# Optimization experiments

Measured on AMD Instinct MI355X. Metric: run time of the kernel, lower is better.

## Reference

```python
import jax, jax.numpy as jnp
import numpy as np

EPS = 1e-5
NUM_HEADS = 8


def _conv(x, w, pad, dil=1, groups=1, b=None):
    y = jax.lax.conv_general_dilated(
        x, w, (1, 1), pad, rhs_dilation=(dil, dil),
        dimension_numbers=('NCHW', 'OIHW', 'NCHW'), feature_group_count=groups)
    if b is not None:
        y = y + b[None, :, None, None]
    return y


def _bn_relu(x, gamma, beta):
    # BatchNorm2d in training mode: batch statistics over (N,H,W) per channel
    mu = x.mean(axis=(0, 2, 3), keepdims=True)
    var = x.var(axis=(0, 2, 3), keepdims=True)
    y = (x - mu) / jnp.sqrt(var + EPS) * gamma[None, :, None, None] + beta[None, :, None, None]
    return jax.nn.relu(y)


def _ln(x, w, b):
    # WithBias LayerNorm over channel dim (to_3d makes C the last axis)
    mu = x.mean(axis=1, keepdims=True)
    var = x.var(axis=1, keepdims=True)
    return (x - mu) / jnp.sqrt(var + EPS) * w[None, :, None, None] + b[None, :, None, None]


def _l2n(t):
    # torch F.normalize: x / max(||x||_2, 1e-12)
    return t / jnp.maximum(jnp.linalg.norm(t, axis=-1, keepdims=True), 1e-12)


def _forward(x, ln_w, ln_b, wd1, gd1, bd1, wd2, gd2, bd2, wd3, gd3, bd3,
             w_out1, w1, b1, w2, b2, w3, b3, w4, b4, w5, b5, w6, b6, w_out2):
    B, C, H, W = x.shape
    head, ch = NUM_HEADS, C // NUM_HEADS
    x1 = _ln(x, ln_w, ln_b)
    # dilated dense-conv branch (DConv2d = conv -> BN -> ReLU), dilations [1,6,12]
    x11 = _bn_relu(_conv(x, wd1, ((0, 0), (0, 0))), gd1, bd1)
    x12 = _bn_relu(_conv(x, wd2, ((6, 6), (6, 6)), dil=6), gd2, bd2)
    x13 = _bn_relu(_conv(x, wd3, ((12, 12), (12, 12)), dil=12), gd3, bd3)
    out2 = _conv(x11 + x12 + x13, w_out1, ((0, 0), (0, 0))) + x
    # six depthwise conv branches, summed
    att = (_conv(x1, w1, ((0, 0), (2, 2)), groups=C, b=b1)
           + _conv(x1, w2, ((2, 2), (0, 0)), groups=C, b=b2)
           + _conv(x1, w3, ((0, 0), (0, 0)), groups=C, b=b3)
           + _conv(x1, w4, ((1, 1), (1, 1)), groups=C, b=b4)
           + _conv(x1, w5, ((0, 0), (3, 3)), groups=C, b=b5)
           + _conv(x1, w6, ((3, 3), (0, 0)), groups=C, b=b6))
    out1 = _conv(att, w_out2, ((0, 0), (0, 0)))

    def r_hwc(t):  # b (head c) h w -> b head h (w c)
        return t.reshape(B, head, ch, H, W).transpose(0, 1, 3, 4, 2).reshape(B, head, H, W * ch)

    def r_whc(t):  # b (head c) h w -> b head w (h c)
        return t.reshape(B, head, ch, H, W).transpose(0, 1, 4, 3, 2).reshape(B, head, W, H * ch)

    k1 = _l2n(r_hwc(out1))
    v1 = r_hwc(out1)
    k2 = _l2n(r_whc(out2))
    v2 = r_whc(out2)
    q2 = _l2n(r_whc(out1))
    q1 = _l2n(r_whc(out2))
    A1 = jax.nn.softmax(q1 @ jnp.swapaxes(k1, -2, -1), axis=-1)  # [B,head,W,H]
    out3 = A1 @ v1 + q1
    A2 = jax.nn.softmax(q2 @ jnp.swapaxes(k2, -2, -1), axis=-1)
    out4 = A2 @ v2 + q2
    # b head h (w c) -> b (head c) h w
    o3 = out3.reshape(B, head, H, W, ch).transpose(0, 1, 4, 2, 3).reshape(B, C, H, W)
    # b head w (h c) -> b (head c) h w
    o4 = out4.reshape(B, head, W, H, ch).transpose(0, 1, 4, 3, 2).reshape(B, C, H, W)
    return _conv(o3, w_out2, ((0, 0), (0, 0))) + _conv(o4, w_out2, ((0, 0), (0, 0))) + x


def setup_inputs() -> dict:
    key = jax.random.key(0)
    ks = jax.random.split(key, 16)
    B, C, H, W = 8, 128, 128, 128

    def rn(k, shape, s):
        return jax.random.normal(k, shape, jnp.float32) * s

    inp = {}
    inp['x'] = jax.random.normal(ks[0], (B, C, H, W), jnp.float32)
    inp['ln_w'] = jnp.ones((C,), jnp.float32)
    inp['ln_b'] = jnp.zeros((C,), jnp.float32)
    inp['wd1'] = rn(ks[1], (C, C, 1, 1), 0.1)
    inp['gd1'] = jnp.ones((C,), jnp.float32)
    inp['bd1'] = jnp.zeros((C,), jnp.float32)
    inp['wd2'] = rn(ks[2], (C, C, 3, 3), 0.04)
    inp['gd2'] = jnp.ones((C,), jnp.float32)
    inp['bd2'] = jnp.zeros((C,), jnp.float32)
    inp['wd3'] = rn(ks[3], (C, C, 3, 3), 0.04)
    inp['gd3'] = jnp.ones((C,), jnp.float32)
    inp['bd3'] = jnp.zeros((C,), jnp.float32)
    inp['w_out1'] = rn(ks[4], (C, C, 1, 1), 0.09)
    inp['w1'] = rn(ks[5], (C, 1, 1, 5), 0.3)
    inp['b1'] = jnp.zeros((C,), jnp.float32)
    inp['w2'] = rn(ks[6], (C, 1, 5, 1), 0.3)
    inp['b2'] = jnp.zeros((C,), jnp.float32)
    inp['w3'] = rn(ks[7], (C, 1, 1, 1), 0.5)
    inp['b3'] = jnp.zeros((C,), jnp.float32)
    inp['w4'] = rn(ks[8], (C, 1, 3, 3), 0.2)
    inp['b4'] = jnp.zeros((C,), jnp.float32)
    inp['w5'] = rn(ks[9], (C, 1, 1, 7), 0.25)
    inp['b5'] = jnp.zeros((C,), jnp.float32)
    inp['w6'] = rn(ks[10], (C, 1, 7, 1), 0.25)
    inp['b6'] = jnp.zeros((C,), jnp.float32)
    inp['w_out2'] = rn(ks[11], (C, C, 1, 1), 0.09)
    return inp


def reference(x, ln_w, ln_b, wd1, gd1, bd1, wd2, gd2, bd2, wd3, gd3, bd3,
              w_out1, w1, b1, w2, b2, w3, b3, w4, b4, w5, b5, w6, b6, w_out2):
    return _forward(x, ln_w, ln_b, wd1, gd1, bd1, wd2, gd2, bd2, wd3, gd3, bd3,
                    w_out1, w1, b1, w2, b2, w3, b3, w4, b4, w5, b5, w6, b6, w_out2)
```

## Files before the change

kernel.cpp:

```cpp
#include <hip/hip_runtime.h>

#define Bb 8
#define Cc 128
#define Hh 128
#define Ww 128
#define HW 16384
#define CHW (Cc*HW)
#define NHW (Bb*HW)
#define CH 16
#define EPS 1e-5f
#define NSLICE 16

typedef __attribute__((ext_vector_type(8))) short bf16x8;
typedef __attribute__((ext_vector_type(4))) float f32x4;

static __device__ __forceinline__ short f2b(float f) {
  unsigned u = __float_as_uint(f);
  unsigned lsb = (u >> 16) & 1;
  return (short)((u + 0x7fffu + lsb) >> 16);
}
static __device__ __forceinline__ float b2f(short s) {
  return __uint_as_float(((unsigned)(unsigned short)s) << 16);
}

static __device__ __forceinline__ void stats_epilogue(
    float* __restrict__ statp, f32x4 acc[4][4], int co0, int quad, int lm)
{
  statp += (blockIdx.x & (NSLICE-1)) * 768;
  #pragma unroll
  for (int i = 0; i < 4; ++i) {
    f32x4 s = acc[i][0] + acc[i][1] + acc[i][2] + acc[i][3];
    f32x4 q = acc[i][0]*acc[i][0] + acc[i][1]*acc[i][1]
            + acc[i][2]*acc[i][2] + acc[i][3]*acc[i][3];
    #pragma unroll
    for (int m = 1; m < 16; m <<= 1) {
      #pragma unroll
      for (int e = 0; e < 4; ++e) {
        s[e] += __shfl_xor(s[e], m);
        q[e] += __shfl_xor(q[e], m);
      }
    }
    if (lm == 0) {
      int co = co0 + i*16 + quad*4;
      #pragma unroll
      for (int e = 0; e < 4; ++e) {
        atomicAdd(&statp[co + e], s[e]);
        atomicAdd(&statp[128 + co + e], q[e]);
      }
    }
  }
}

__global__ __launch_bounds__(256) void k_ln(const float* __restrict__ x,
    const float* __restrict__ g, const float* __restrict__ be,
    float* __restrict__ y)
{
  int p = blockIdx.x*256 + threadIdx.x;
  int b = p >> 14, hw = p & 16383;
  const float* xp = x + (long)b*CHW + hw;
  float s = 0.f, q = 0.f;
  for (int c = 0; c < Cc; ++c) { float v = xp[c*HW]; s += v; q += v*v; }
  float mu = s * (1.f/Cc);
  float var = q * (1.f/Cc) - mu*mu;
  float rstd = rsqrtf(var + EPS);
  float* yp = y + (long)b*CHW + hw;
  for (int c = 0; c < Cc; ++c) {
    float v = xp[c*HW];
    yp[c*HW] = (v - mu) * rstd * g[c] + be[c];
  }
}

__global__ __launch_bounds__(256) void k_reorg3b(const float* __restrict__ Wt, short* __restrict__ out)
{
  int idx = blockIdx.x*256 + threadIdx.x;
  int tap = idx >> 14, r = idx & 16383;
  out[idx] = f2b(Wt[r*9 + tap]);
}

__global__ __launch_bounds__(256) void k_cast(const float* __restrict__ in, short* __restrict__ out)
{
  int i = blockIdx.x*256 + threadIdx.x;
  out[i] = f2b(in[i]);
}

__global__ __launch_bounds__(256) void k_zero(float* p, int n)
{
  int i = blockIdx.x*256 + threadIdx.x;
  if (i < n) p[i] = 0.f;
}

__global__ __launch_bounds__(256) void k_nhwc(const float* __restrict__ in, short* __restrict__ out)
{
  __shared__ float Ls[32][33];
  int bid = blockIdx.x;
  int hwt = bid & 511, c4 = (bid>>9)&3, b = bid>>11;
  int hw0 = hwt << 5, c0 = c4 << 5;
  int t = threadIdx.x;
  int hl = t & 31, cl = t >> 5;
  const float* p = in + (long)b*CHW + hw0;
  for (int r = cl; r < 32; r += 8)
    Ls[r][hl] = p[(long)(c0+r)*HW + hl];
  __syncthreads();
  short* q = out + ((long)b*HW + hw0)*Cc + c0;
  int ccl = t & 31, hl0 = t >> 5;
  for (int r = hl0; r < 32; r += 8)
    q[(long)r*Cc + ccl] = f2b(Ls[ccl][r]);
}

__global__ __launch_bounds__(256,2) void k_mconv(const short* __restrict__ X,
    const short* __restrict__ W, float* __restrict__ Y, int k3, int dil,
    float* __restrict__ statp)
{
  __shared__ short Ws[128*136];
  __shared__ short Xs[152*136];
  int b = blockIdx.x >> 7, h = blockIdx.x & 127;
  int t = threadIdx.x;
  int wave = t >> 6, lane = t & 63;
  int co0 = (wave >> 1) << 6, sp0 = (wave & 1) << 6;
  int lm = lane & 15, quad = lane >> 4;
  f32x4 acc[4][4];
  #pragma unroll
  for (int i = 0; i < 4; ++i)
    #pragma unroll
    for (int j = 0; j < 4; ++j) acc[i][j] = (f32x4){0.f,0.f,0.f,0.f};
  int half = k3 >> 1;

  {
    f32x4 z = {0.f,0.f,0.f,0.f};
    for (int i = t; i < 408; i += 256) {
      int r = i / 17, o = i - r*17;
      int row = r < 12 ? r : r + 128;
      *(f32x4*)(Xs + row*136 + o*8) = z;
    }
  }

  for (int kh = 0; kh < k3; ++kh) {
    int hs = h + (kh - half)*dil;
    if ((unsigned)hs >= (unsigned)Hh) continue;
    __syncthreads();
    {
      const short* xr = X + ((long)(b*Hh + hs)*Ww)*Cc;
      #pragma unroll
      for (int it = 0; it < 8; ++it) {
        int i = t + it*256;
        int row = i >> 4, off = (i & 15) << 3;
        *(f32x4*)(Xs + (12 + row)*136 + off) = *(const f32x4*)(xr + (long)row*Cc + off);
      }
    }
    for (int kw = 0; kw < k3; ++kw) {
      int dw = (kw - half)*dil;
      if (kw) __syncthreads();
      {
        const short* wt = W + (kh*k3 + kw)*16384;
        #pragma unroll
        for (int it = 0; it < 8; ++it) {
          int i = t + it*256;
          int row = i >> 4, off = (i & 15) << 3;
          *(f32x4*)(Ws + row*136 + off) = *(const f32x4*)(wt + (long)row*128 + off);
        }
      }
      __syncthreads();
      int xrow0 = 12 + dw + sp0;
      for (int kc = 0; kc < 4; ++kc) {
        int k0 = kc << 5;
        bf16x8 af[4], bfr[4];
        #pragma unroll
        for (int i = 0; i < 4; ++i)
          af[i] = *(const bf16x8*)(Ws + (co0 + i*16 + lm)*136 + k0 + quad*8);
        #pragma unroll
        for (int j = 0; j < 4; ++j)
          bfr[j] = *(const bf16x8*)(Xs + (xrow0 + j*16 + lm)*136 + k0 + quad*8);
        #pragma unroll
        for (int i = 0; i < 4; ++i)
          #pragma unroll
          for (int j = 0; j < 4; ++j)
            acc[i][j] = __builtin_amdgcn_mfma_f32_16x16x32_bf16(af[i], bfr[j], acc[i][j], 0, 0, 0);
      }
    }
  }
  float* yb = Y + ((long)(b*Hh + h)*Ww)*Cc;
  #pragma unroll
  for (int i = 0; i < 4; ++i) {
    int co = co0 + i*16 + quad*4;
    #pragma unroll
    for (int j = 0; j < 4; ++j) {
      int wc = sp0 + j*16 + lm;
      *(f32x4*)(yb + (long)wc*Cc + co) = acc[i][j];
    }
  }
  if (statp) stats_epilogue(statp, acc, co0, quad, lm);
}

__global__ __launch_bounds__(256,4) void k_mconv1(const short* __restrict__ X,
    const short* __restrict__ W, const float* __restrict__ res,
    float* __restrict__ Y, int nhwc, float* __restrict__ statp)
{
  __shared__ short Ws[128*136];
  int b = blockIdx.x >> 7, h = blockIdx.x & 127;
  int t = threadIdx.x;
  int wave = t >> 6, lane = t & 63;
  int co0 = (wave >> 1) << 6, sp0 = (wave & 1) << 6;
  int lm = lane & 15, quad = lane >> 4;
  #pragma unroll
  for (int it = 0; it < 8; ++it) {
    int i = t + it*256;
    int row = i >> 4, off = (i & 15) << 3;
    *(f32x4*)(Ws + row*136 + off) = *(const f32x4*)(W + (long)row*128 + off);
  }
  f32x4 acc[4][4];
  #pragma unroll
  for (int i = 0; i < 4; ++i)
    #pragma unroll
    for (int j = 0; j < 4; ++j) acc[i][j] = (f32x4){0.f,0.f,0.f,0.f};
  const short* xr = X + ((long)(b*Hh + h)*Ww)*Cc;
  __syncthreads();
  #pragma unroll
  for (int kc = 0; kc < 4; ++kc) {
    int k0 = kc << 5;
    bf16x8 af[4], bfr[4];
    #pragma unroll
    for (int j = 0; j < 4; ++j)
      bfr[j] = *(const bf16x8*)(xr + (long)(sp0 + j*16 + lm)*Cc + k0 + quad*8);
    #pragma unroll
    for (int i = 0; i < 4; ++i)
      af[i] = *(const bf16x8*)(Ws + (co0 + i*16 + lm)*136 + k0 + quad*8);
    #pragma unroll
    for (int i = 0; i < 4; ++i)
      #pragma unroll
      for (int j = 0; j < 4; ++j)
        acc[i][j] = __builtin_amdgcn_mfma_f32_16x16x32_bf16(af[i], bfr[j], acc[i][j], 0, 0, 0);
  }
  if (nhwc) {
    float* yb = Y + ((long)(b*Hh + h)*Ww)*Cc;
    #pragma unroll
    for (int i = 0; i < 4; ++i) {
      int co = co0 + i*16 + quad*4;
      #pragma unroll
      for (int j = 0; j < 4; ++j) {
        int wc = sp0 + j*16 + lm;
        *(f32x4*)(yb + (long)wc*Cc + co) = acc[i][j];
      }
    }
    if (statp) stats_epilogue(statp, acc, co0, quad, lm);
  } else {
    __syncthreads();
    float* scr = (float*)Ws + wave*320;
    int co_l = lane >> 2, wq = (lane & 3) << 2;
    #pragma unroll
    for (int i = 0; i < 4; ++i) {
      #pragma unroll
      for (int j = 0; j < 4; ++j) {
        #pragma unroll
        for (int r = 0; r < 4; ++r)
          scr[(quad*4 + r)*20 + lm] = acc[i][j][r];
        f32x4 vv = *(f32x4*)(scr + co_l*20 + wq);
        int co = co0 + i*16 + co_l;
        int wc = sp0 + j*16 + wq;
        long idx = ((long)(b*Cc + co)*Hh + h)*Ww + wc;
        if (res) vv += *(const f32x4*)(res + idx);
        *(f32x4*)(Y + idx) = vv;
      }
    }
  }
}

__global__ __launch_bounds__(128) void k_bnfin(const float* __restrict__ stats,
    const float* __restrict__ g1, const float* __restrict__ be1,
    const float* __restrict__ g2, const float* __restrict__ be2,
    const float* __restrict__ g3, const float* __restrict__ be3,
    float* __restrict__ so)
{
  int c = threadIdx.x;
  const float inv = 1.f/(float)NHW;
  const float* gs[3] = {g1, g2, g3};
  const float* bs[3] = {be1, be2, be3};
  #pragma unroll
  for (int tsel = 0; tsel < 3; ++tsel) {
    float su = 0.f, qu = 0.f;
    for (int sl = 0; sl < NSLICE; ++sl) {
      su += stats[sl*768 + tsel*256 + c];
      qu += stats[sl*768 + tsel*256 + 128 + c];
    }
    float mu = su*inv;
    float var = qu*inv - mu*mu;
    float s = rsqrtf(var + EPS)*gs[tsel][c];
    so[tsel*256 + c] = s;
    so[tsel*256 + 128 + c] = bs[tsel][c] - mu*s;
  }
}

__global__ __launch_bounds__(256) void k_bnapply(const float* __restrict__ y1,
    const float* __restrict__ y2, const float* __restrict__ y3,
    const float* __restrict__ so, short* __restrict__ sb)
{
  long e = ((long)blockIdx.x*256 + threadIdx.x) * 8;
  int c = (int)(e & 127);
  f32x4 s1a = *(const f32x4*)(so + c),        s1b = *(const f32x4*)(so + c + 4);
  f32x4 o1a = *(const f32x4*)(so + 128 + c),  o1b = *(const f32x4*)(so + 132 + c);
  f32x4 s2a = *(const f32x4*)(so + 256 + c),  s2b = *(const f32x4*)(so + 260 + c);
  f32x4 o2a = *(const f32x4*)(so + 384 + c),  o2b = *(const f32x4*)(so + 388 + c);
  f32x4 s3a = *(const f32x4*)(so + 512 + c),  s3b = *(const f32x4*)(so + 516 + c);
  f32x4 o3a = *(const f32x4*)(so + 640 + c),  o3b = *(const f32x4*)(so + 644 + c);
  f32x4 v1a = *(const f32x4*)(y1 + e), v1b = *(const f32x4*)(y1 + e + 4);
  f32x4 v2a = *(const f32x4*)(y2 + e), v2b = *(const f32x4*)(y2 + e + 4);
  f32x4 v3a = *(const f32x4*)(y3 + e), v3b = *(const f32x4*)(y3 + e + 4);
  float r[8];
  #pragma unroll
  for (int k = 0; k < 4; ++k) {
    r[k] = fmaxf(fmaf(v1a[k], s1a[k], o1a[k]), 0.f)
         + fmaxf(fmaf(v2a[k], s2a[k], o2a[k]), 0.f)
         + fmaxf(fmaf(v3a[k], s3a[k], o3a[k]), 0.f);
    r[4+k] = fmaxf(fmaf(v1b[k], s1b[k], o1b[k]), 0.f)
           + fmaxf(fmaf(v2b[k], s2b[k], o2b[k]), 0.f)
           + fmaxf(fmaf(v3b[k], s3b[k], o3b[k]), 0.f);
  }
  int4 o;
  o.x = ((int)(unsigned short)f2b(r[1])<<16) | (unsigned short)f2b(r[0]);
  o.y = ((int)(unsigned short)f2b(r[3])<<16) | (unsigned short)f2b(r[2]);
  o.z = ((int)(unsigned short)f2b(r[5])<<16) | (unsigned short)f2b(r[4]);
  o.w = ((int)(unsigned short)f2b(r[7])<<16) | (unsigned short)f2b(r[6]);
  *(int4*)(sb + e) = o;
}

__global__ __launch_bounds__(256) void k_dw2(const float* __restrict__ X,
    const float* __restrict__ w1, const float* __restrict__ b1,
    const float* __restrict__ w2, const float* __restrict__ b2,
    const float* __restrict__ w3, const float* __restrict__ b3,
    const float* __restrict__ w4, const float* __restrict__ b4,
    const float* __restrict__ w5, const float* __restrict__ b5,
    const float* __restrict__ w6, const float* __restrict__ b6,
    float* __restrict__ Y)
{
  __shared__ float Ls[38][136];
  int bid = blockIdx.x;
  int tile = bid & 3, plane = bid >> 2;
  int c = plane & 127;
  int h0 = tile << 5;
  int t = threadIdx.x;

  float hcoef[7], vcoef[7], k9[9];
  #pragma unroll
  for (int d = 0; d < 7; ++d) { hcoef[d] = w5[c*7+d]; vcoef[d] = w6[c*7+d]; }
  #pragma unroll
  for (int d = 1; d < 6; ++d) { hcoef[d] += w1[c*5+d-1]; vcoef[d] += w2[c*5+d-1]; }
  hcoef[3] += w3[c];
  #pragma unroll
  for (int k = 0; k < 9; ++k) k9[k] = w4[c*9+k];
  float bias = b1[c]+b2[c]+b3[c]+b4[c]+b5[c]+b6[c];

  const float* xp = X + (long)plane*HW;

  f32x4* lz = (f32x4*)&Ls[0][0];
  for (int i = t; i < 1292; i += 256) lz[i] = (f32x4){0.f,0.f,0.f,0.f};
  __syncthreads();
  for (int i = t; i < 1216; i += 256) {
    int r = i >> 5, cg = (i & 31) << 2;
    int h = h0 - 3 + r;
    if ((unsigned)h < 128u)
      *(f32x4*)&Ls[r][4 + cg] = *(const f32x4*)(xp + h*128 + cg);
  }
  __syncthreads();

  int g = t & 31, rs = t >> 5;
  int w0 = g << 2;
  float* Yp = Y + (long)plane*HW;

  for (int ro = 0; ro < 4; ++ro) {
    int lr = rs + (ro << 3);
    int R = lr + 3;
    f32x4 a0 = *(const f32x4*)&Ls[R][w0];
    f32x4 a1 = *(const f32x4*)&Ls[R][w0+4];
    f32x4 a2 = *(const f32x4*)&Ls[R][w0+8];
    f32x4 u0 = *(const f32x4*)&Ls[R-1][w0];
    f32x4 u1 = *(const f32x4*)&Ls[R-1][w0+4];
    f32x4 u2 = *(const f32x4*)&Ls[R-1][w0+8];
    f32x4 d0 = *(const f32x4*)&Ls[R+1][w0];
    f32x4 d1 = *(const f32x4*)&Ls[R+1][w0+4];
    f32x4 d2 = *(const f32x4*)&Ls[R+1][w0+8];
    f32x4 v3u = *(const f32x4*)&Ls[R-3][w0+4];
    f32x4 v2u = *(const f32x4*)&Ls[R-2][w0+4];
    f32x4 v2d = *(const f32x4*)&Ls[R+2][w0+4];
    f32x4 v3d = *(const f32x4*)&Ls[R+3][w0+4];

    float cr[12], ur[12], dr[12];
    #pragma unroll
    for (int k = 0; k < 4; ++k) {
      cr[k] = a0[k]; cr[4+k] = a1[k]; cr[8+k] = a2[k];
      ur[k] = u0[k]; ur[4+k] = u1[k]; ur[8+k] = u2[k];
      dr[k] = d0[k]; dr[4+k] = d1[k]; dr[8+k] = d2[k];
    }

    f32x4 o;
    #pragma unroll
    for (int j = 0; j < 4; ++j) {
      float acc = bias;
      #pragma unroll
      for (int d = 0; d < 7; ++d) acc = fmaf(hcoef[d], cr[j+d+1], acc);
      acc = fmaf(vcoef[0], v3u[j], acc);
      acc = fmaf(vcoef[1], v2u[j], acc);
      acc = fmaf(vcoef[2], ur[j+4], acc);
      acc = fmaf(vcoef[3], cr[j+4], acc);
      acc = fmaf(vcoef[4], dr[j+4], acc);
      acc = fmaf(vcoef[5], v2d[j], acc);
      acc = fmaf(vcoef[6], v3d[j], acc);
      #pragma unroll
      for (int kw = 0; kw < 3; ++kw) {
        acc = fmaf(k9[kw],   ur[j+3+kw], acc);
        acc = fmaf(k9[3+kw], cr[j+3+kw], acc);
        acc = fmaf(k9[6+kw], dr[j+3+kw], acc);
      }
      o[j] = acc;
    }
    *(f32x4*)(Yp + (h0 + lr)*128 + w0) = o;
  }
}

__global__ __launch_bounds__(256) void k_normh(const float* __restrict__ out1, float* __restrict__ invn)
{
  __shared__ float red[256];
  int bid = blockIdx.x;
  int h = bid & 127; int bh = bid >> 7;
  int b = bh >> 3, hd = bh & 7;
  const float* p = out1 + ((long)(b*Cc + hd*CH)*Hh + h)*Ww;
  float s = 0.f;
  for (int e = threadIdx.x; e < 2048; e += 256) {
    int c = e >> 7, w = e & 127;
    float v = p[(long)c*HW + w];
    s += v*v;
  }
  red[threadIdx.x] = s; __syncthreads();
  for (int st = 128; st > 0; st >>= 1) {
    if (threadIdx.x < st) red[threadIdx.x] += red[threadIdx.x+st];
    __syncthreads();
  }
  if (threadIdx.x == 0) invn[bid] = 1.f/fmaxf(sqrtf(red[0]), 1e-12f);
}

__global__ __launch_bounds__(256) void k_normw_part(const float* __restrict__ out1,
    const float* __restrict__ out2, float* __restrict__ acc1, float* __restrict__ acc2)
{
  __shared__ float red[4][256];
  int bid = blockIdx.x;
  int c = bid & 15, bh = (bid >> 4) & 63, tsel = bid >> 10;
  int b = bh >> 3, hd = bh & 7;
  const float* p = (tsel ? out2 : out1) + (long)(b*Cc + hd*CH + c)*HW;
  int t = threadIdx.x;
  const float4* p4 = (const float4*)p;
  float s0 = 0.f, s1 = 0.f, s2 = 0.f, s3 = 0.f;
  for (int i = t; i < 4096; i += 256) {
    float4 v = p4[i];
    s0 += v.x*v.x; s1 += v.y*v.y; s2 += v.z*v.z; s3 += v.w*v.w;
  }
  red[0][t] = s0; red[1][t] = s1; red[2][t] = s2; red[3][t] = s3;
  __syncthreads();
  if (t < 128) {
    int j = t >> 5;
    int g = t & 31;
    float tot = 0.f;
    #pragma unroll
    for (int r = 0; r < 8; ++r) tot += red[j][g + r*32];
    atomicAdd((tsel ? acc2 : acc1) + bh*128 + g*4 + j, tot);
  }
}

__global__ __launch_bounds__(256) void k_finw(float* __restrict__ p)
{
  int i = blockIdx.x*256 + threadIdx.x;
  float v = p[i];
  p[i] = 1.f/fmaxf(sqrtf(v), 1e-12f);
}

__global__ __launch_bounds__(256) void k_t12(const float* __restrict__ out1,
    const float* __restrict__ out2, short* __restrict__ out1T, short* __restrict__ out2T)
{
  __shared__ float Ls[32][33];
  int bid = blockIdx.x;
  int wt = bid&3, ht=(bid>>2)&3, c=(bid>>4)&127, b=(bid>>11)&7, src=bid>>14;
  const float* in = (src ? out2 : out1) + (long)(b*128+c)*16384;
  short* outp = (src ? out2T : out1T) + ((long)(b*8 + (c>>4))*128)*2048 + (c&15)*128;
  int h0 = ht*32, w0 = wt*32;
  int t = threadIdx.x, li = t&31, r0 = t>>5;
  for (int r = r0; r < 32; r += 8)
    Ls[r][li] = in[(h0+r)*128 + w0 + li];
  __syncthreads();
  for (int r = r0; r < 32; r += 8)
    outp[(long)(w0+r)*2048 + h0 + li] = f2b(Ls[li][r]);
}

__global__ __launch_bounds__(256) void k_h12(const float* __restrict__ out1,
    const float* __restrict__ out2, short* __restrict__ out1H, short* __restrict__ out2H)
{
  int bid = blockIdx.x;
  int src = bid >> 13;
  long e = ((long)(bid & 8191)*256 + threadIdx.x) * 8;
  const float* p;
  short* dst;
  if (src) { p = out2 + e; dst = out2H + e; }
  else {
    int c = (int)((e>>7)&15), h = (int)((e>>11)&127), hd=(int)((e>>18)&7), b=(int)(e>>21);
    int pp = (int)(e & 127);
    p = out1 + (((long)(b*128 + hd*16 + c)*128 + h)*128 + pp);
    dst = out1H + e;
  }
  int4 o;
  o.x = ((int)(unsigned short)f2b(p[1])<<16) | (unsigned short)f2b(p[0]);
  o.y = ((int)(unsigned short)f2b(p[3])<<16) | (unsigned short)f2b(p[2]);
  o.z = ((int)(unsigned short)f2b(p[5])<<16) | (unsigned short)f2b(p[4]);
  o.w = ((int)(unsigned short)f2b(p[7])<<16) | (unsigned short)f2b(p[6]);
  *(int4*)dst = o;
}

__global__ __launch_bounds__(256) void k_attnS_m(
    const short* __restrict__ out1T, const short* __restrict__ out2T,
    const short* __restrict__ out1H,
    const float* __restrict__ invn1h, const float* __restrict__ invn1w,
    const float* __restrict__ invn2w,
    short* __restrict__ A1b, short* __restrict__ A2b)
{
  __shared__ short As[128*72];
  __shared__ short Bs[128*72];
  int bid = blockIdx.x;
  int type = bid >> 6, bh = bid & 63;
  const short* Aop = (type ? out1T : out2T) + (long)bh*262144;
  const short* Bop = (type ? out2T : out1H) + (long)bh*262144;
  const float* invrow = (type ? invn1w : invn2w) + bh*128;
  const float* invcol = (type ? invn2w : invn1h) + bh*128;
  short* Aout = (type ? A2b : A1b) + (long)bh*16384;
  int t = threadIdx.x;
  int wave = t >> 6, lane = t & 63, lm = lane & 15, quad = lane >> 4;
  int m0 = wave << 5;
  f32x4 acc[2][8];
  #pragma unroll
  for (int i = 0; i < 2; ++i)
    #pragma unroll
    for (int j = 0; j < 8; ++j) acc[i][j] = (f32x4){0.f,0.f,0.f,0.f};
  for (int kc = 0; kc < 32; ++kc) {
    int k0 = kc << 6;
    __syncthreads();
    #pragma unroll
    for (int i = 0; i < 4; ++i) {
      int e = t + i*256;
      int row = e >> 3, off = (e & 7) << 3;
      *(float4*)(As + row*72 + off) = *(const float4*)(Aop + (long)row*2048 + k0 + off);
      *(float4*)(Bs + row*72 + off) = *(const float4*)(Bop + (long)row*2048 + k0 + off);
    }
    __syncthreads();
    #pragma unroll
    for (int ks = 0; ks < 64; ks += 32) {
      bf16x8 af[2], bfj[8];
      #pragma unroll
      for (int i = 0; i < 2; ++i)
        af[i] = *(const bf16x8*)(As + (m0 + i*16 + lm)*72 + ks + quad*8);
      #pragma unroll
      for (int j = 0; j < 8; ++j)
        bfj[j] = *(const bf16x8*)(Bs + (j*16 + lm)*72 + ks + quad*8);
      #pragma unroll
      for (int i = 0; i < 2; ++i)
        #pragma unroll
        for (int j = 0; j < 8; ++j)
          acc[i][j] = __builtin_amdgcn_mfma_f32_16x16x32_bf16(af[i], bfj[j], acc[i][j], 0, 0, 0);
    }
  }
  float colv[8];
  #pragma unroll
  for (int j = 0; j < 8; ++j) colv[j] = invcol[j*16 + lm];
  #pragma unroll
  for (int i = 0; i < 2; ++i) {
    #pragma unroll
    for (int r = 0; r < 4; ++r) {
      int row = m0 + i*16 + quad*4 + r;
      float rs = invrow[row];
      float sv[8];
      float mx = -1e30f;
      #pragma unroll
      for (int j = 0; j < 8; ++j) {
        sv[j] = acc[i][j][r] * rs * colv[j];
        mx = fmaxf(mx, sv[j]);
      }
      mx = fmaxf(mx, __shfl_xor(mx, 1));
      mx = fmaxf(mx, __shfl_xor(mx, 2));
      mx = fmaxf(mx, __shfl_xor(mx, 4));
      mx = fmaxf(mx, __shfl_xor(mx, 8));
      float sum = 0.f;
      #pragma unroll
      for (int j = 0; j < 8; ++j) { sv[j] = __expf(sv[j] - mx); sum += sv[j]; }
      sum += __shfl_xor(sum, 1);
      sum += __shfl_xor(sum, 2);
      sum += __shfl_xor(sum, 4);
      sum += __shfl_xor(sum, 8);
      float inv = 1.f/sum;
      #pragma unroll
      for (int j = 0; j < 8; ++j)
        Aout[row*128 + j*16 + lm] = f2b(sv[j]*inv);
    }
  }
}

__global__ __launch_bounds__(256) void k_o34f(
    const short* __restrict__ A1b, const short* __restrict__ out1T,
    const short* __restrict__ out1H, const float* __restrict__ invn1w,
    const short* __restrict__ out2H, const short* __restrict__ A2b,
    const float* __restrict__ out2, const float* __restrict__ invn2w,
    float* __restrict__ o34)
{
  __shared__ short As[128*72];
  __shared__ short Bs[128*72];
  int bid = blockIdx.x;
  int cf = bid & 127, b = bid >> 7;
  int hd = cf >> 4, c = cf & 15;
  int bh = b*8 + hd;
  const short* A0 = A1b + (long)bh*16384;
  const short* B0 = out1T + (long)bh*262144 + c*128;
  const short* A1_ = out2H + (long)(b*128 + cf)*16384;
  const short* B1_ = A2b + (long)bh*16384;
  const short* R = out1H + (long)bh*262144 + c*128;
  const float* o2p = out2 + (long)(b*128 + cf)*16384;
  const float* inw1 = invn1w + bh*128;
  const float* inw2 = invn2w + bh*128;
  float* O = o34 + (long)(b*128 + cf)*16384;
  int t = threadIdx.x;
  int wave = t >> 6, lane = t & 63, lm = lane & 15, quad = lane >> 4;
  int m0 = (wave >> 1) << 6, n0 = (wave & 1) << 6;
  f32x4 acc[4][4];
  #pragma unroll
  for (int i = 0; i < 4; ++i)
    #pragma unroll
    for (int j = 0; j < 4; ++j) acc[i][j] = (f32x4){0.f,0.f,0.f,0.f};
  for (int g = 0; g < 4; ++g) {
    const short* Asrc = (g < 2) ? A0 : A1_;
    const short* Bsrc = (g < 2) ? B0 : B1_;
    long Bst = (g < 2) ? 2048 : 128;
    int k0 = (g & 1) << 6;
    __syncthreads();
    #pragma unroll
    for (int i = 0; i < 4; ++i) {
      int e = t + i*256;
      int row = e >> 3, off = (e & 7) << 3;
      *(float4*)(As + row*72 + off) = *(const float4*)(Asrc + (long)row*128 + k0 + off);
      *(float4*)(Bs + row*72 + off) = *(const float4*)(Bsrc + (long)row*Bst + k0 + off);
    }
    __syncthreads();
    #pragma unroll
    for (int ks = 0; ks < 64; ks += 32) {
      bf16x8 af[4], bfj[4];
      #pragma unroll
      for (int i = 0; i < 4; ++i)
        af[i] = *(const bf16x8*)(As + (m0 + i*16 + lm)*72 + ks + quad*8);
      #pragma unroll
      for (int j = 0; j < 4; ++j)
        bfj[j] = *(const bf16x8*)(Bs + (n0 + j*16 + lm)*72 + ks + quad*8);
      #pragma unroll
      for (int i = 0; i < 4; ++i)
        #pragma unroll
        for (int j = 0; j < 4; ++j)
          acc[i][j] = __builtin_amdgcn_mfma_f32_16x16x32_bf16(af[i], bfj[j], acc[i][j], 0, 0, 0);
    }
  }
  float inwv[4];
  #pragma unroll
  for (int j = 0; j < 4; ++j) inwv[j] = inw1[n0 + j*16 + lm];
  #pragma unroll
  for (int i = 0; i < 4; ++i) {
    int row0 = m0 + i*16 + quad*4;
    f32x4 iv2 = *(const f32x4*)(inw2 + row0);
    #pragma unroll
    for (int j = 0; j < 4; ++j) {
      int col = n0 + j*16 + lm;
      f32x4 vq = *(const f32x4*)(o2p + (long)col*128 + row0);
      #pragma unroll
      for (int r = 0; r < 4; ++r)
        acc[i][j][r] += b2f(R[(long)(row0 + r)*2048 + col]) * inwv[j]
                      + vq[r] * iv2[r];
    }
  }
  __syncthreads();
  float* scr = (float*)As + wave*320;
  int co_l = lane >> 2, wq = (lane & 3) << 2;
  #pragma unroll
  for (int i = 0; i < 4; ++i) {
    #pragma unroll
    for (int j = 0; j < 4; ++j) {
      #pragma unroll
      for (int r = 0; r < 4; ++r)
        scr[(quad*4 + r)*20 + lm] = acc[i][j][r];
      f32x4 vv = *(f32x4*)(scr + co_l*20 + wq);
      *(f32x4*)(O + (long)(m0 + i*16 + co_l)*128 + n0 + j*16 + wq) = vv;
    }
  }
}

extern "C" void kernel_launch(void* const* d_in, const int* in_sizes, int n_in,
                              void* d_out, int out_size, void* d_ws, size_t ws_size,
                              hipStream_t stream)
{
  const float* x    = (const float*)d_in[0];
  const float* ln_w = (const float*)d_in[1];
  const float* ln_b = (const float*)d_in[2];
  const float* wd1  = (const float*)d_in[3];
  const float* gd1  = (const float*)d_in[4];
  const float* bd1  = (const float*)d_in[5];
  const float* wd2  = (const float*)d_in[6];
  const float* gd2  = (const float*)d_in[7];
  const float* bd2  = (const float*)d_in[8];
  const float* wd3  = (const float*)d_in[9];
  const float* gd3  = (const float*)d_in[10];
  const float* bd3  = (const float*)d_in[11];
  const float* w_out1 = (const float*)d_in[12];
  const float* w1 = (const float*)d_in[13]; const float* b1 = (const float*)d_in[14];
  const float* w2 = (const float*)d_in[15]; const float* b2 = (const float*)d_in[16];
  const float* w3 = (const float*)d_in[17]; const float* b3 = (const float*)d_in[18];
  const float* w4 = (const float*)d_in[19]; const float* b4 = (const float*)d_in[20];
  const float* w5 = (const float*)d_in[21]; const float* b5 = (const float*)d_in[22];
  const float* w6 = (const float*)d_in[23]; const float* b6 = (const float*)d_in[24];
  const float* w_out2 = (const float*)d_in[25];
  float* out = (float*)d_out;

  const long SLAB = 16777216L;
  float* buf0 = (float*)d_ws;
  float* buf1 = buf0 + SLAB;
  float* buf2 = buf1 + SLAB;
  float* dbuf = out;
  float* stats = buf2 + SLAB;
  float* invn1h = stats + NSLICE*768;
  float* invn1w = invn1h + 8192;
  float* invn2w = invn1w + 8192;
  short* wb2  = (short*)(invn2w + 8192);
  short* wb3  = wb2 + 147456;
  short* wb1  = wb3 + 147456;
  short* wbo1 = wb1 + 16384;
  short* wbo2 = wbo1 + 16384;
  short* A1b  = wbo2 + 16384;
  short* A2b  = A1b + 1048576;
  float* bnso = (float*)(A2b + 1048576);

  short* xb = (short*)buf0;
  short* sb = (short*)buf0;
  short* ab = (short*)buf1;
  short* out1T = (short*)dbuf;
  short* out2T = out1T + 16777216;
  short* out1H = (short*)buf1;
  short* out2H = out1H + 16777216;
  short* ob = (short*)buf1;

  k_zero<<<48, 256, 0, stream>>>(stats, NSLICE*768);
  k_zero<<<64, 256, 0, stream>>>(invn1w, 16384);
  k_reorg3b<<<576, 256, 0, stream>>>(wd2, wb2);
  k_reorg3b<<<576, 256, 0, stream>>>(wd3, wb3);
  k_cast<<<64, 256, 0, stream>>>(wd1, wb1);
  k_cast<<<64, 256, 0, stream>>>(w_out1, wbo1);
  k_cast<<<64, 256, 0, stream>>>(w_out2, wbo2);

  k_nhwc<<<16384, 256, 0, stream>>>(x, xb);
  k_mconv1<<<1024, 256, 0, stream>>>(xb, wb1, nullptr, buf1, 1, stats);
  k_mconv<<<1024, 256, 0, stream>>>(xb, wb2, buf2, 3, 6, stats + 256);
  k_mconv<<<1024, 256, 0, stream>>>(xb, wb3, dbuf, 3, 12, stats + 512);
  k_bnfin<<<1, 128, 0, stream>>>(stats, gd1, bd1, gd2, bd2, gd3, bd3, bnso);
  k_bnapply<<<8192, 256, 0, stream>>>(buf1, buf2, dbuf, bnso, sb);
  k_mconv1<<<1024, 256, 0, stream>>>(sb, wbo1, x, buf2, 0, nullptr);
  k_ln<<<512, 256, 0, stream>>>(x, ln_w, ln_b, buf0);
  k_dw2<<<4096, 256, 0, stream>>>(buf0, w1,b1,w2,b2,w3,b3,w4,b4,w5,b5,w6,b6, dbuf);
  k_nhwc<<<16384, 256, 0, stream>>>(dbuf, ab);
  k_mconv1<<<1024, 256, 0, stream>>>(ab, wbo2, nullptr, buf0, 0, nullptr);
  k_normh<<<8192, 256, 0, stream>>>(buf0, invn1h);
  k_normw_part<<<2048, 256, 0, stream>>>(buf0, buf2, invn1w, invn2w);
  k_finw<<<64, 256, 0, stream>>>(invn1w);
  k_t12<<<32768, 256, 0, stream>>>(buf0, buf2, out1T, out2T);
  k_h12<<<16384, 256, 0, stream>>>(buf0, buf2, out1H, out2H);
  k_attnS_m<<<128, 256, 0, stream>>>(out1T, out2T, out1H,
                                     invn1h, invn1w, invn2w, A1b, A2b);
  k_o34f<<<1024, 256, 0, stream>>>(A1b, out1T, out1H, invn1w,
                                   out2H, A2b, buf2, invn2w, buf0);
  k_nhwc<<<16384, 256, 0, stream>>>(buf0, ob);
  k_mconv1<<<1024, 256, 0, stream>>>(ob, wbo2, x, out, 0, nullptr);
}
```

Before: 795.4 us.

## Emit bf16 intermediates and fuse transpose/head-reorder kernels to cut memory traffic

The depthwise-conv kernel and the attention-output kernel now write bf16 instead of fp32, and a new bf16-to-bf16 NHWC transpose replaces the fp32-input transpose for those two paths. This halves the bytes written and re-read for these intermediates. The separate T and H reorganization kernels are merged into one kernel that reads each fp32 tile once and writes both layouts, removing one full pass over out1/out2. Rounding to bf16 earlier slightly changes numerics, although those tensors were already converted to bf16 before the next GEMM.

```diff
diff --git a/kernel.cpp b/kernel.cpp
--- a/kernel.cpp
+++ b/kernel.cpp
@@ -105,6 +105,24 @@
   int ccl = t & 31, hl0 = t >> 5;
   for (int r = hl0; r < 32; r += 8)
     q[(long)r*Cc + ccl] = f2b(Ls[ccl][r]);
+}
+
+__global__ __launch_bounds__(256) void k_nhwcb(const short* __restrict__ in, short* __restrict__ out)
+{
+  __shared__ short Ls[32][34];
+  int bid = blockIdx.x;
+  int hwt = bid & 511, c4 = (bid>>9)&3, b = bid>>11;
+  int hw0 = hwt << 5, c0 = c4 << 5;
+  int t = threadIdx.x;
+  int hl = t & 31, cl = t >> 5;
+  const short* p = in + (long)b*CHW + hw0;
+  for (int r = cl; r < 32; r += 8)
+    Ls[r][hl] = p[(long)(c0+r)*HW + hl];
+  __syncthreads();
+  short* q = out + ((long)b*HW + hw0)*Cc + c0;
+  int ccl = t & 31, hl0 = t >> 5;
+  for (int r = hl0; r < 32; r += 8)
+    q[(long)r*Cc + ccl] = Ls[ccl][r];
 }
 
 __global__ __launch_bounds__(256,2) void k_mconv(const short* __restrict__ X,
@@ -329,7 +347,7 @@
     const float* __restrict__ w4, const float* __restrict__ b4,
     const float* __restrict__ w5, const float* __restrict__ b5,
     const float* __restrict__ w6, const float* __restrict__ b6,
-    float* __restrict__ Y)
+    short* __restrict__ Y)
 {
   __shared__ float Ls[38][136];
   int bid = blockIdx.x;
@@ -363,7 +381,7 @@
 
   int g = t & 31, rs = t >> 5;
   int w0 = g << 2;
-  float* Yp = Y + (long)plane*HW;
+  short* Yp = Y + (long)plane*HW;
 
   for (int ro = 0; ro < 4; ++ro) {
     int lr = rs + (ro << 3);
@@ -390,7 +408,7 @@
       dr[k] = d0[k]; dr[4+k] = d1[k]; dr[8+k] = d2[k];
     }
 
-    f32x4 o;
+    float o[4];
     #pragma unroll
     for (int j = 0; j < 4; ++j) {
       float acc = bias;
@@ -411,7 +429,10 @@
       }
       o[j] = acc;
     }
-    *(f32x4*)(Yp + (h0 + lr)*128 + w0) = o;
+    int2 ov;
+    ov.x = ((int)(unsigned short)f2b(o[1])<<16) | (unsigned short)f2b(o[0]);
+    ov.y = ((int)(unsigned short)f2b(o[3])<<16) | (unsigned short)f2b(o[2]);
+    *(int2*)(Yp + (h0 + lr)*128 + w0) = ov;
   }
 }
 
@@ -470,44 +491,29 @@
   p[i] = 1.f/fmaxf(sqrtf(v), 1e-12f);
 }
 
-__global__ __launch_bounds__(256) void k_t12(const float* __restrict__ out1,
-    const float* __restrict__ out2, short* __restrict__ out1T, short* __restrict__ out2T)
+__global__ __launch_bounds__(256) void k_thx(const float* __restrict__ out1,
+    const float* __restrict__ out2,
+    short* __restrict__ out1T, short* __restrict__ out2T,
+    short* __restrict__ out1H, short* __restrict__ out2H)
 {
   __shared__ float Ls[32][33];
   int bid = blockIdx.x;
   int wt = bid&3, ht=(bid>>2)&3, c=(bid>>4)&127, b=(bid>>11)&7, src=bid>>14;
   const float* in = (src ? out2 : out1) + (long)(b*128+c)*16384;
-  short* outp = (src ? out2T : out1T) + ((long)(b*8 + (c>>4))*128)*2048 + (c&15)*128;
+  long tbase = ((long)(b*8 + (c>>4))*128)*2048 + (c&15)*128;
+  short* pT = (src ? out2T : out1T) + tbase;
+  short* pH; long hstr;
+  if (src) { pH = out2H + (long)(b*128+c)*16384; hstr = 128; }
+  else     { pH = out1H + tbase;                 hstr = 2048; }
   int h0 = ht*32, w0 = wt*32;
   int t = threadIdx.x, li = t&31, r0 = t>>5;
   for (int r = r0; r < 32; r += 8)
     Ls[r][li] = in[(h0+r)*128 + w0 + li];
   __syncthreads();
-  for (int r = r0; r < 32; r += 8)
-    outp[(long)(w0+r)*2048 + h0 + li] = f2b(Ls[li][r]);
-}
-
-__global__ __launch_bounds__(256) void k_h12(const float* __restrict__ out1,
-    const float* __restrict__ out2, short* __restrict__ out1H, short* __restrict__ out2H)
-{
-  int bid = blockIdx.x;
-  int src = bid >> 13;
-  long e = ((long)(bid & 8191)*256 + threadIdx.x) * 8;
-  const float* p;
-  short* dst;
-  if (src) { p = out2 + e; dst = out2H + e; }
-  else {
-    int c = (int)((e>>7)&15), h = (int)((e>>11)&127), hd=(int)((e>>18)&7), b=(int)(e>>21);
-    int pp = (int)(e & 127);
-    p = out1 + (((long)(b*128 + hd*16 + c)*128 + h)*128 + pp);
-    dst = out1H + e;
-  }
-  int4 o;
-  o.x = ((int)(unsigned short)f2b(p[1])<<16) | (unsigned short)f2b(p[0]);
-  o.y = ((int)(unsigned short)f2b(p[3])<<16) | (unsigned short)f2b(p[2]);
-  o.z = ((int)(unsigned short)f2b(p[5])<<16) | (unsigned short)f2b(p[4]);
-  o.w = ((int)(unsigned short)f2b(p[7])<<16) | (unsigned short)f2b(p[6]);
-  *(int4*)dst = o;
+  for (int r = r0; r < 32; r += 8) {
+    pT[(long)(w0+r)*2048 + h0 + li] = f2b(Ls[li][r]);
+    pH[(long)(h0+r)*hstr + w0 + li] = f2b(Ls[r][li]);
+  }
 }
 
 __global__ __launch_bounds__(256) void k_attnS_m(
@@ -601,7 +607,7 @@
     const short* __restrict__ out1H, const float* __restrict__ invn1w,
     const short* __restrict__ out2H, const short* __restrict__ A2b,
     const float* __restrict__ out2, const float* __restrict__ invn2w,
-    float* __restrict__ o34)
+    short* __restrict__ o34b)
 {
   __shared__ short As[128*72];
   __shared__ short Bs[128*72];
@@ -617,7 +623,7 @@
   const float* o2p = out2 + (long)(b*128 + cf)*16384;
   const float* inw1 = invn1w + bh*128;
   const float* inw2 = invn2w + bh*128;
-  float* O = o34 + (long)(b*128 + cf)*16384;
+  short* O = o34b + (long)(b*128 + cf)*16384;
   int t = threadIdx.x;
   int wave = t >> 6, lane = t & 63, lm = lane & 15, quad = lane >> 4;
   int m0 = (wave >> 1) << 6, n0 = (wave & 1) << 6;
@@ -684,7 +690,10 @@
       for (int r = 0; r < 4; ++r)
         scr[(quad*4 + r)*20 + lm] = acc[i][j][r];
       f32x4 vv = *(f32x4*)(scr + co_l*20 + wq);
-      *(f32x4*)(O + (long)(m0 + i*16 + co_l)*128 + n0 + j*16 + wq) = vv;
+      int2 ov;
+      ov.x = ((int)(unsigned short)f2b(vv[1])<<16) | (unsigned short)f2b(vv[0]);
+      ov.y = ((int)(unsigned short)f2b(vv[3])<<16) | (unsigned short)f2b(vv[2]);
+      *(int2*)(O + (long)(m0 + i*16 + co_l)*128 + n0 + j*16 + wq) = ov;
     }
   }
 }
@@ -735,11 +744,13 @@
 
   short* xb = (short*)buf0;
   short* sb = (short*)buf0;
+  short* attb = (short*)dbuf;
   short* ab = (short*)buf1;
   short* out1T = (short*)dbuf;
   short* out2T = out1T + 16777216;
   short* out1H = (short*)buf1;
   short* out2H = out1H + 16777216;
+  short* o34b = (short*)buf0;
   short* ob = (short*)buf1;
 
   k_zero<<<48, 256, 0, stream>>>(stats, NSLICE*768);
@@ -758,18 +769,17 @@
   k_bnapply<<<8192, 256, 0, stream>>>(buf1, buf2, dbuf, bnso, sb);
   k_mconv1<<<1024, 256, 0, stream>>>(sb, wbo1, x, buf2, 0, nullptr);
   k_ln<<<512, 256, 0, stream>>>(x, ln_w, ln_b, buf0);
-  k_dw2<<<4096, 256, 0, stream>>>(buf0, w1,b1,w2,b2,w3,b3,w4,b4,w5,b5,w6,b6, dbuf);
-  k_nhwc<<<16384, 256, 0, stream>>>(dbuf, ab);
+  k_dw2<<<4096, 256, 0, stream>>>(buf0, w1,b1,w2,b2,w3,b3,w4,b4,w5,b5,w6,b6, attb);
+  k_nhwcb<<<16384, 256, 0, stream>>>(attb, ab);
   k_mconv1<<<1024, 256, 0, stream>>>(ab, wbo2, nullptr, buf0, 0, nullptr);
   k_normh<<<8192, 256, 0, stream>>>(buf0, invn1h);
   k_normw_part<<<2048, 256, 0, stream>>>(buf0, buf2, invn1w, invn2w);
   k_finw<<<64, 256, 0, stream>>>(invn1w);
-  k_t12<<<32768, 256, 0, stream>>>(buf0, buf2, out1T, out2T);
-  k_h12<<<16384, 256, 0, stream>>>(buf0, buf2, out1H, out2H);
+  k_thx<<<32768, 256, 0, stream>>>(buf0, buf2, out1T, out2T, out1H, out2H);
   k_attnS_m<<<128, 256, 0, stream>>>(out1T, out2T, out1H,
                                      invn1h, invn1w, invn2w, A1b, A2b);
   k_o34f<<<1024, 256, 0, stream>>>(A1b, out1T, out1H, invn1w,
-                                   out2H, A2b, buf2, invn2w, buf0);
-  k_nhwc<<<16384, 256, 0, stream>>>(buf0, ob);
+                                   out2H, A2b, buf2, invn2w, o34b);
+  k_nhwcb<<<16384, 256, 0, stream>>>(o34b, ob);
   k_mconv1<<<1024, 256, 0, stream>>>(ob, wbo2, x, out, 0, nullptr);
 }
```

Result: faster. 758.8 us (-4.6%).
